# Kernel optimization log

Measured on AMD Instinct MI355X. Metric: run time of the kernel, lower is better.

Reference implementation:

```python
import jax, jax.numpy as jnp
import numpy as np

# BERT-base geometry
B, N, H, DH = 4, 512, 12, 64
HID = H * DH            # 768
E = 65536               # total edges (~avg degree 32)
NREL = 64               # relation vocabulary


def setup_inputs() -> dict:
    key = jax.random.key(0)
    ks = jax.random.split(key, 12)
    node_states = jax.random.normal(ks[0], (B, N, HID), jnp.float32)
    b = jax.random.randint(ks[1], (E,), 0, B)
    hn = jax.random.randint(ks[2], (E,), 0, N)
    tn = jax.random.randint(ks[3], (E,), 0, N)
    r = jax.random.randint(ks[4], (E,), 0, NREL)
    edge_indices = jnp.stack([b, hn, tn, r]).astype(jnp.int32)  # (4, E)
    node_type_ids = jnp.zeros((B, N), jnp.int32)  # unused by this subclass
    sc = 0.02
    Wq = jax.random.normal(ks[5], (HID, HID), jnp.float32) * sc
    bq = jnp.zeros((HID,), jnp.float32)
    Wk = jax.random.normal(ks[6], (HID, HID), jnp.float32) * sc
    bk = jnp.zeros((HID,), jnp.float32)
    Wv = jax.random.normal(ks[7], (HID, HID), jnp.float32) * sc
    bv = jnp.zeros((HID,), jnp.float32)
    # relation matrix embeddings: one (DH, DH) matrix per relation id
    rel_emb = jnp.eye(DH, dtype=jnp.float32)[None] + jax.random.normal(ks[8], (NREL, DH, DH), jnp.float32) * sc
    return {"node_states": node_states, "edge_indices": edge_indices,
            "node_type_ids": node_type_ids, "Wq": Wq, "bq": bq,
            "Wk": Wk, "bk": bk, "Wv": Wv, "bv": bv, "rel_emb": rel_emb}


def reference(node_states, edge_indices, node_type_ids, Wq, bq, Wk, bk, Wv, bv, rel_emb):
    Bq, Nn, hid = node_states.shape
    # dense QKV projections (torch Linear: y = x @ W^T + b)
    Q = node_states @ Wq.T + bq
    K = node_states @ Wk.T + bk
    V = (node_states @ Wv.T + bv).reshape(Bq, Nn, H, DH)  # (B,N,H,D)
    be, he, te, re = edge_indices  # each (E,)
    # per-edge gathers
    Qe = Q[be, he].reshape(-1, H, DH)   # (E,H,D)
    Ke = K[be, te].reshape(-1, H, DH)   # (E,H,D)
    Re = rel_emb[re]                     # (E,D,D) relation matrix per edge
    # Q projected through relation matrix, then inner product with K per head
    Qp = jnp.einsum('ehd,edk->ehk', Qe, Re)
    logits = jnp.einsum('ehd,ehd->eh', Qp, Ke) / jnp.sqrt(jnp.float32(DH))  # (E,H)
    # sparse softmax over tail nodes: segment = (batch, head_node)
    seg = be * Nn + he
    nseg = Bq * Nn
    m = jax.ops.segment_max(logits, seg, num_segments=nseg)      # (BN,H)
    ex = jnp.exp(logits - m[seg])
    denom = jax.ops.segment_sum(ex, seg, num_segments=nseg)      # (BN,H)
    p = ex / denom[seg]                                          # (E,H)
    # dropout prob = 0.0 (deterministic reference)
    # aggregate: out[b,i,h,:] = sum_edges p_e * V[b, tail_e, h, :]
    contrib = p[:, :, None] * V[be, te]                          # (E,H,D)
    out = jax.ops.segment_sum(contrib, seg, num_segments=nseg)   # (BN,H,D)
    return out.reshape(Bq, Nn, H * DH)
```

## Files before the change

### kernel.cpp

```cpp
#include <hip/hip_runtime.h>
#include <hip/hip_bf16.h>

#define NB   4
#define NN   512
#define NH   12
#define DHD  64
#define HID  768
#define NE   65536
#define NSEG 2048
#define NREL 64
#define NSUB 32
#define NRSUB (NREL * NSUB)
#define LGS  16

typedef short bf16x8 __attribute__((ext_vector_type(8)));
typedef float f32x4  __attribute__((ext_vector_type(4)));
typedef unsigned short u16x8 __attribute__((ext_vector_type(8)));

__device__ __forceinline__ unsigned short f2bf(float f) {
    __hip_bfloat16 h = __float2bfloat16(f);
    return *reinterpret_cast<unsigned short*>(&h);
}
__device__ __forceinline__ float bf2f(unsigned short s) {
    return __int_as_float(((int)s) << 16);
}
__device__ __forceinline__ void load_lds16(const void* g, void* l) {
    __builtin_amdgcn_global_load_lds(
        (const __attribute__((address_space(1))) unsigned int*)g,
        (__attribute__((address_space(3))) unsigned int*)l, 16, 0, 0);
}

__global__ __launch_bounds__(256) void zero_kernel(int* __restrict__ counters)
{
    ((int4*)counters)[blockIdx.x * 256 + threadIdx.x] = (int4){0, 0, 0, 0};
}

#define NX4 ((2048 * 768) / 4)
#define NW4 ((768 * 768) / 4)
#define NCAST ((NX4 + 3 * NW4) / 256)
__global__ __launch_bounds__(256) void cast_hist_kernel(
    const float* __restrict__ X, const float* __restrict__ Wq,
    const float* __restrict__ Wk, const float* __restrict__ Wv,
    unsigned short* __restrict__ Xh, unsigned short* __restrict__ Wh,
    const int* __restrict__ ei,
    int* __restrict__ count, int* __restrict__ rcount2)
{
    if (blockIdx.x >= NCAST) {
        const int e = (blockIdx.x - NCAST) * 256 + threadIdx.x;
        const int b  = ei[e];
        const int hn = ei[NE + e];
        const int rr = ei[3 * NE + e];
        const int sub = (e >> 8) & (NSUB - 1);
        atomicAdd(&count[b * NN + hn], 1);
        atomicAdd(&rcount2[rr * NSUB + sub], 1);
        return;
    }
    const int i = blockIdx.x * 256 + threadIdx.x;
    float4 v;
    ushort4* dst;
    if (i < NX4) {
        v = ((const float4*)X)[i];
        dst = &((ushort4*)Xh)[i];
    } else {
        const int j = i - NX4;
        const float* W = (j < NW4) ? Wq : ((j < 2 * NW4) ? Wk : Wv);
        const int jj = (j < NW4) ? j : ((j < 2 * NW4) ? j - NW4 : j - 2 * NW4);
        v = ((const float4*)W)[jj];
        dst = &((ushort4*)Wh)[j];
    }
    ushort4 r;
    r.x = f2bf(v.x); r.y = f2bf(v.y); r.z = f2bf(v.z); r.w = f2bf(v.w);
    *dst = r;
}

__global__ __launch_bounds__(256) void qkv_mfma(
    const unsigned short* __restrict__ Xh, const unsigned short* __restrict__ Wh,
    const float* __restrict__ bq, const float* __restrict__ bk,
    const float* __restrict__ bv,
    unsigned short* __restrict__ Qh, unsigned short* __restrict__ Kh,
    float* __restrict__ Vo)
{
    const int z = blockIdx.z;
    const unsigned short* W = Wh + (size_t)z * (768 * 768);
    const float* bias = (z == 0) ? bq : ((z == 1) ? bk : bv);

    const int n0 = blockIdx.x * 128;
    const int m0 = blockIdx.y * 64;
    const int tid  = threadIdx.x;
    const int lane = tid & 63;
    const int wave = tid >> 6;
    const int wm = wave >> 1, wn = wave & 1;

    __shared__ __align__(16) char smem[64 * 132 * 4];
    unsigned short* As = (unsigned short*)smem;
    unsigned short* Bs = (unsigned short*)(smem + 8192);
    float* Cs = (float*)smem;

    f32x4 acc[2][4];
    #pragma unroll
    for (int a = 0; a < 2; ++a)
        #pragma unroll
        for (int b = 0; b < 4; ++b) acc[a][b] = (f32x4){0.f, 0.f, 0.f, 0.f};

    const int ml = lane & 15;
    const int q4 = lane >> 4;

    for (int k0 = 0; k0 < HID; k0 += 64) {
        __syncthreads();
        #pragma unroll
        for (int i = 0; i < 2; ++i) {
            const int slotb = i * 256 + wave * 64;
            const int idx = slotb + lane;
            const int row = idx >> 3;
            const int kq  = (idx & 7) ^ (row & 7);
            load_lds16(Xh + (size_t)(m0 + row) * HID + k0 + kq * 8,
                       As + slotb * 8);
        }
        #pragma unroll
        for (int i = 0; i < 4; ++i) {
            const int slotb = i * 256 + wave * 64;
            const int idx = slotb + lane;
            const int row = idx >> 3;
            const int kq  = (idx & 7) ^ (row & 7);
            load_lds16(W + (size_t)(n0 + row) * HID + k0 + kq * 8,
                       Bs + slotb * 8);
        }
        __syncthreads();

        #pragma unroll
        for (int ks = 0; ks < 2; ++ks) {
            bf16x8 af[2], bfr[4];
            #pragma unroll
            for (int t = 0; t < 2; ++t) {
                const int ar = wm * 32 + t * 16 + ml;
                const int ac = (ks * 4 + q4) ^ (ar & 7);
                af[t] = *(const bf16x8*)(As + ar * 64 + ac * 8);
            }
            #pragma unroll
            for (int t = 0; t < 4; ++t) {
                const int br = wn * 64 + t * 16 + ml;
                const int bc = (ks * 4 + q4) ^ (br & 7);
                bfr[t] = *(const bf16x8*)(Bs + br * 64 + bc * 8);
            }
            #pragma unroll
            for (int mt = 0; mt < 2; ++mt)
                #pragma unroll
                for (int nt = 0; nt < 4; ++nt)
                    acc[mt][nt] = __builtin_amdgcn_mfma_f32_16x16x32_bf16(
                        af[mt], bfr[nt], acc[mt][nt], 0, 0, 0);
        }
    }

    __syncthreads();
    #pragma unroll
    for (int mt = 0; mt < 2; ++mt)
        #pragma unroll
        for (int nt = 0; nt < 4; ++nt)
            #pragma unroll
            for (int rg = 0; rg < 4; ++rg)
                Cs[(wm * 32 + mt * 16 + q4 * 4 + rg) * 132 +
                   wn * 64 + nt * 16 + ml] = acc[mt][nt][rg];
    __syncthreads();

    #pragma unroll
    for (int it = 0; it < 4; ++it) {
        const int id  = tid + it * 256;
        const int row = id >> 4;
        const int cg  = id & 15;
        const float* cp = Cs + row * 132 + cg * 8;
        const float4 cA = *(const float4*)cp;
        const float4 cB = *(const float4*)(cp + 4);
        const float* bp = bias + n0 + cg * 8;
        const float4 bA = *(const float4*)bp;
        const float4 bB = *(const float4*)(bp + 4);
        const size_t o = (size_t)(m0 + row) * HID + n0 + cg * 8;
        if (z == 2) {
            float4 rA, rB;
            rA.x = cA.x + bA.x; rA.y = cA.y + bA.y;
            rA.z = cA.z + bA.z; rA.w = cA.w + bA.w;
            rB.x = cB.x + bB.x; rB.y = cB.y + bB.y;
            rB.z = cB.z + bB.z; rB.w = cB.w + bB.w;
            *(float4*)&Vo[o]     = rA;
            *(float4*)&Vo[o + 4] = rB;
        } else {
            u16x8 r;
            r[0] = f2bf(cA.x + bA.x); r[1] = f2bf(cA.y + bA.y);
            r[2] = f2bf(cA.z + bA.z); r[3] = f2bf(cA.w + bA.w);
            r[4] = f2bf(cB.x + bB.x); r[5] = f2bf(cB.y + bB.y);
            r[6] = f2bf(cB.z + bB.z); r[7] = f2bf(cB.w + bB.w);
            unsigned short* Y = (z == 0) ? Qh : Kh;
            *(u16x8*)&Y[o] = r;
        }
    }
}

__global__ void scan2_kernel(const int* __restrict__ cntA, int* __restrict__ ofsA,
                             const int* __restrict__ cntB, int* __restrict__ ofsB)
{
    const int* cnt = blockIdx.x ? cntB : cntA;
    int* ofs       = blockIdx.x ? ofsB : ofsA;
    __shared__ int buf[256];
    const int tid = threadIdx.x;
    int local[8];
    int s = 0;
    #pragma unroll
    for (int i = 0; i < 8; ++i) { local[i] = cnt[tid * 8 + i]; s += local[i]; }
    buf[tid] = s;
    __syncthreads();
    for (int off = 1; off < 256; off <<= 1) {
        const int v = (tid >= off) ? buf[tid - off] : 0;
        __syncthreads();
        buf[tid] += v;
        __syncthreads();
    }
    int run = buf[tid] - s;
    #pragma unroll
    for (int i = 0; i < 8; ++i) { ofs[tid * 8 + i] = run; run += local[i]; }
    if (tid == 255) ofs[2048] = run;
}

__global__ void scatter_kernel(const int* __restrict__ ei, const int* __restrict__ offs,
                               int* __restrict__ cursor,
                               const int* __restrict__ rofs2, int* __restrict__ rcursor2,
                               int* __restrict__ s_te, int* __restrict__ s_seg,
                               int* __restrict__ r_pos)
{
    const int e = blockIdx.x * 256 + threadIdx.x;
    const int b  = ei[e];
    const int hn = ei[NE + e];
    const int tn = ei[2 * NE + e];
    const int rr = ei[3 * NE + e];
    const int sub = (e >> 8) & (NSUB - 1);
    const int seg = b * NN + hn;
    const int pos = offs[seg] + atomicAdd(&cursor[seg], 1);
    s_te[pos]  = tn;
    s_seg[pos] = seg;
    const int rb = rr * NSUB + sub;
    const int rj = atomicAdd(&rcursor2[rb], 1);
    r_pos[rofs2[rb] + rj] = pos;
}

#define RLY 32
__global__ __launch_bounds__(256) void rel_logits(
    const unsigned short* __restrict__ Qh, const unsigned short* __restrict__ Kh,
    const float* __restrict__ rel,
    const int* __restrict__ rofs2, const int* __restrict__ r_pos,
    const int* __restrict__ s_te, const int* __restrict__ s_seg,
    float* __restrict__ Lg)
{
    const int r = blockIdx.x;
    const int rstart = rofs2[r * NSUB];
    const int rows = (rofs2[(r + 1) * NSUB] - rstart) * NH;
    if ((int)blockIdx.y * 256 >= rows) return;
    const int tid = threadIdx.x;
    const int lane = tid & 63;
    const int wave = tid >> 6;

    __shared__ int qb[256], kb[256], oi[256];
    __shared__ float QpS[4][16][68];

    bf16x8 bfrag[2][4];
    {
        const float* Rg = rel + (size_t)r * 4096;
        const int q4 = lane >> 4, n = lane & 15;
        #pragma unroll
        for (int ks = 0; ks < 2; ++ks)
            #pragma unroll
            for (int nt = 0; nt < 4; ++nt) {
                bf16x8 f;
                #pragma unroll
                for (int j = 0; j < 8; ++j)
                    f[j] = (short)f2bf(Rg[(ks * 32 + q4 * 8 + j) * 64 + nt * 16 + n]);
                bfrag[ks][nt] = f;
            }
    }

    for (int t0 = blockIdx.y * 256; t0 < rows; t0 += RLY * 256) {
        __syncthreads();
        {
            const int rowid = t0 + tid;
            if (rowid < rows) {
                const int el = rowid / 12;
                const int h  = rowid - el * 12;
                const int pos = r_pos[rstart + el];
                const int seg = s_seg[pos];
                const int te  = s_te[pos];
                const int b   = seg >> 9;
                qb[tid] = seg * HID + h * 64;
                kb[tid] = (b * NN + te) * HID + h * 64;
                oi[tid] = pos * LGS + h;
            } else { qb[tid] = 0; kb[tid] = 0; oi[tid] = -1; }
        }
        __syncthreads();

        for (int g = wave; g < 16; g += 4) {
            const int m = lane & 15, q4 = lane >> 4;
            const int qbase = qb[g * 16 + m];
            f32x4 cfr[4] = {{0,0,0,0},{0,0,0,0},{0,0,0,0},{0,0,0,0}};
            #pragma unroll
            for (int ks = 0; ks < 2; ++ks) {
                const bf16x8 afr = *(const bf16x8*)(Qh + qbase + ks * 32 + q4 * 8);
                #pragma unroll
                for (int nt = 0; nt < 4; ++nt)
                    cfr[nt] = __builtin_amdgcn_mfma_f32_16x16x32_bf16(
                        afr, bfrag[ks][nt], cfr[nt], 0, 0, 0);
            }
            #pragma unroll
            for (int nt = 0; nt < 4; ++nt)
                #pragma unroll
                for (int rg = 0; rg < 4; ++rg)
                    QpS[wave][q4 * 4 + rg][nt * 16 + m] = cfr[nt][rg];

            const int rw = lane >> 2, ch = (lane & 3) * 16;
            const int rowid2 = g * 16 + rw;
            const int kbase = kb[rowid2];
            const bf16x8 k0 = *(const bf16x8*)(Kh + kbase + ch);
            const bf16x8 k1 = *(const bf16x8*)(Kh + kbase + ch + 8);
            float s = 0.f;
            #pragma unroll
            for (int i = 0; i < 8; ++i) {
                s = fmaf(QpS[wave][rw][ch + i],     bf2f((unsigned short)k0[i]), s);
                s = fmaf(QpS[wave][rw][ch + 8 + i], bf2f((unsigned short)k1[i]), s);
            }
            s += __shfl_xor(s, 1, 64);
            s += __shfl_xor(s, 2, 64);
            if ((lane & 3) == 0) {
                const int o = oi[rowid2];
                if (o >= 0) Lg[o] = s * 0.125f;
            }
        }
    }
}

__global__ __launch_bounds__(256) void seg_softmax_agg(
    const float* __restrict__ V, const float* __restrict__ Lg,
    const int* __restrict__ offs, const int* __restrict__ s_te,
    float* __restrict__ out)
{
    const int seg  = blockIdx.x;
    const int tid  = threadIdx.x;
    const int lane = tid & 63;
    const int w    = tid >> 6;
    const int start = offs[seg];
    const int cnt   = offs[seg + 1] - start;
    const int browbase = seg & ~(NN - 1);

    __shared__ int   te_s[64];
    __shared__ float pv[4][3][64];

    float l0 = 0.f, l1 = 0.f, l2 = 0.f;
    float acc0 = 0.f, acc1 = 0.f, acc2 = 0.f;

    for (int c0 = 0; c0 < cnt; c0 += 64) {
        const int cc = min(64, cnt - c0);
        __syncthreads();
        if (tid < cc) te_s[tid] = s_te[start + c0 + tid];
        __syncthreads();

        float p0 = 0.f, p1 = 0.f, p2 = 0.f;
        if (lane < cc) {
            const float* Lp = Lg + (size_t)(start + c0 + lane) * LGS;
            p0 = __expf(Lp[w]); p1 = __expf(Lp[4 + w]); p2 = __expf(Lp[8 + w]);
        }
        float s0 = p0, s1 = p1, s2 = p2;
        #pragma unroll
        for (int o = 1; o < 64; o <<= 1) {
            s0 += __shfl_xor(s0, o, 64);
            s1 += __shfl_xor(s1, o, 64);
            s2 += __shfl_xor(s2, o, 64);
        }
        l0 += s0; l1 += s1; l2 += s2;
        pv[w][0][lane] = p0; pv[w][1][lane] = p1; pv[w][2][lane] = p2;

        for (int j = 0; j < cc; ++j) {
            const float* __restrict__ Vr =
                V + (size_t)(browbase + te_s[j]) * HID + lane;
            acc0 = fmaf(pv[w][0][j], Vr[w * 64],       acc0);
            acc1 = fmaf(pv[w][1][j], Vr[(4 + w) * 64], acc1);
            acc2 = fmaf(pv[w][2][j], Vr[(8 + w) * 64], acc2);
        }
    }

    float* Yo = out + (size_t)seg * HID;
    Yo[tid]       = (l0 > 0.f) ? acc0 / l0 : 0.f;
    Yo[tid + 256] = (l1 > 0.f) ? acc1 / l1 : 0.f;
    Yo[tid + 512] = (l2 > 0.f) ? acc2 / l2 : 0.f;
}

extern "C" void kernel_launch(void* const* d_in, const int* in_sizes, int n_in,
                              void* d_out, int out_size, void* d_ws, size_t ws_size,
                              hipStream_t stream)
{
    const float* X   = (const float*)d_in[0];
    const int*   EI  = (const int*)d_in[1];
    const float* Wq  = (const float*)d_in[3];
    const float* bq  = (const float*)d_in[4];
    const float* Wk  = (const float*)d_in[5];
    const float* bk  = (const float*)d_in[6];
    const float* Wv  = (const float*)d_in[7];
    const float* bv  = (const float*)d_in[8];
    const float* rel = (const float*)d_in[9];
    float* out = (float*)d_out;

    char* p = (char*)d_ws;
    unsigned short* Qh = (unsigned short*)p;  p += (size_t)NSEG * HID * 2;
    unsigned short* Kh = (unsigned short*)p;  p += (size_t)NSEG * HID * 2;
    float* Vb = (float*)p;                    p += (size_t)NSEG * HID * 4;
    unsigned short* Xh = (unsigned short*)p;
    float* Lg = (float*)p;                    p += (size_t)NE * LGS * 4;
    unsigned short* Wh = (unsigned short*)p;  p += (size_t)3 * 768 * 768 * 2;
    int* offs     = (int*)p;                  p += 2052 * 4;
    int* rofs2    = (int*)p;                  p += (NRSUB + 4) * 4;
    int* count    = (int*)p;                  p += NSEG * 4;
    int* cursor   = (int*)p;                  p += NSEG * 4;
    int* rcount2  = (int*)p;                  p += NRSUB * 4;
    int* rcursor2 = (int*)p;                  p += NRSUB * 4;
    int* s_te     = (int*)p;                  p += NE * 4;
    int* s_seg    = (int*)p;                  p += NE * 4;
    int* r_pos    = (int*)p;                  p += NE * 4;

    zero_kernel<<<8, 256, 0, stream>>>(count);
    cast_hist_kernel<<<NCAST + 256, 256, 0, stream>>>(
        X, Wq, Wk, Wv, Xh, Wh, EI, count, rcount2);
    qkv_mfma<<<dim3(HID / 128, (NB * NN) / 64, 3), 256, 0, stream>>>(
        Xh, Wh, bq, bk, bv, Qh, Kh, Vb);

    scan2_kernel<<<2, 256, 0, stream>>>(count, offs, rcount2, rofs2);
    scatter_kernel<<<NE / 256, 256, 0, stream>>>(EI, offs, cursor, rofs2, rcursor2,
                                                 s_te, s_seg, r_pos);

    rel_logits<<<dim3(NREL, RLY), 256, 0, stream>>>(Qh, Kh, rel, rofs2, r_pos,
                                                    s_te, s_seg, Lg);
    seg_softmax_agg<<<NSEG, 256, 0, stream>>>(Vb, Lg, offs, s_te, out);
}
```

Baseline: 176.3 us.

## Fuse prefix scan into scatter, pack seg/tail indices, move exp into logits

Removes the separate two-block scan launch. Every scatter block now recomputes both prefix scans redundantly in shared memory, and block 0 writes the offsets to global memory for later kernels. The per-edge segment and tail indices are packed into one int, so rel_logits does a single gather instead of two. The exp of the logit moves from the softmax kernel into rel_logits. Exponentials are still taken without subtracting the segment max, as before. The cost is 256 blocks each repeating two 2048-entry scans with many barriers, in exchange for one fewer launch and fewer dependent loads.

```diff
diff --git a/kernel.cpp b/kernel.cpp
--- a/kernel.cpp
+++ b/kernel.cpp
@@ -194,50 +194,80 @@
     }
 }
 
-__global__ void scan2_kernel(const int* __restrict__ cntA, int* __restrict__ ofsA,
-                             const int* __restrict__ cntB, int* __restrict__ ofsB)
-{
-    const int* cnt = blockIdx.x ? cntB : cntA;
-    int* ofs       = blockIdx.x ? ofsB : ofsA;
+__global__ __launch_bounds__(256) void scatter_scan_kernel(
+    const int* __restrict__ ei,
+    const int* __restrict__ count, const int* __restrict__ rcount2,
+    int* __restrict__ cursor, int* __restrict__ rcursor2,
+    int* __restrict__ s_te, int* __restrict__ s_pk, int* __restrict__ r_pos,
+    int* __restrict__ offs_g, int* __restrict__ rofs2_g)
+{
+    __shared__ int offs_l[NSEG];
+    __shared__ int rofs_l[NRSUB];
     __shared__ int buf[256];
+    __shared__ int totA;
     const int tid = threadIdx.x;
-    int local[8];
-    int s = 0;
-    #pragma unroll
-    for (int i = 0; i < 8; ++i) { local[i] = cnt[tid * 8 + i]; s += local[i]; }
-    buf[tid] = s;
+
+    {
+        int local[8];
+        int s = 0;
+        #pragma unroll
+        for (int i = 0; i < 8; ++i) { local[i] = count[tid * 8 + i]; s += local[i]; }
+        buf[tid] = s;
+        __syncthreads();
+        for (int off = 1; off < 256; off <<= 1) {
+            const int v = (tid >= off) ? buf[tid - off] : 0;
+            __syncthreads();
+            buf[tid] += v;
+            __syncthreads();
+        }
+        int run = buf[tid] - s;
+        #pragma unroll
+        for (int i = 0; i < 8; ++i) { offs_l[tid * 8 + i] = run; run += local[i]; }
+        if (tid == 255) totA = run;
+        __syncthreads();
+    }
+    {
+        int local[8];
+        int s = 0;
+        #pragma unroll
+        for (int i = 0; i < 8; ++i) { local[i] = rcount2[tid * 8 + i]; s += local[i]; }
+        buf[tid] = s;
+        __syncthreads();
+        for (int off = 1; off < 256; off <<= 1) {
+            const int v = (tid >= off) ? buf[tid - off] : 0;
+            __syncthreads();
+            buf[tid] += v;
+            __syncthreads();
+        }
+        int run = buf[tid] - s;
+        #pragma unroll
+        for (int i = 0; i < 8; ++i) { rofs_l[tid * 8 + i] = run; run += local[i]; }
+        if (blockIdx.x == 0 && tid == 255) rofs2_g[NRSUB] = run;
+    }
     __syncthreads();
-    for (int off = 1; off < 256; off <<= 1) {
-        const int v = (tid >= off) ? buf[tid - off] : 0;
-        __syncthreads();
-        buf[tid] += v;
-        __syncthreads();
-    }
-    int run = buf[tid] - s;
-    #pragma unroll
-    for (int i = 0; i < 8; ++i) { ofs[tid * 8 + i] = run; run += local[i]; }
-    if (tid == 255) ofs[2048] = run;
-}
-
-__global__ void scatter_kernel(const int* __restrict__ ei, const int* __restrict__ offs,
-                               int* __restrict__ cursor,
-                               const int* __restrict__ rofs2, int* __restrict__ rcursor2,
-                               int* __restrict__ s_te, int* __restrict__ s_seg,
-                               int* __restrict__ r_pos)
-{
-    const int e = blockIdx.x * 256 + threadIdx.x;
+
+    if (blockIdx.x == 0) {
+        #pragma unroll
+        for (int i = 0; i < 8; ++i) {
+            offs_g[tid * 8 + i]  = offs_l[tid * 8 + i];
+            rofs2_g[tid * 8 + i] = rofs_l[tid * 8 + i];
+        }
+        if (tid == 255) offs_g[NSEG] = totA;
+    }
+
+    const int e = blockIdx.x * 256 + tid;
     const int b  = ei[e];
     const int hn = ei[NE + e];
     const int tn = ei[2 * NE + e];
     const int rr = ei[3 * NE + e];
     const int sub = (e >> 8) & (NSUB - 1);
     const int seg = b * NN + hn;
-    const int pos = offs[seg] + atomicAdd(&cursor[seg], 1);
-    s_te[pos]  = tn;
-    s_seg[pos] = seg;
+    const int pos = offs_l[seg] + atomicAdd(&cursor[seg], 1);
+    s_te[pos] = tn;
+    s_pk[pos] = (seg << 9) | tn;
     const int rb = rr * NSUB + sub;
     const int rj = atomicAdd(&rcursor2[rb], 1);
-    r_pos[rofs2[rb] + rj] = pos;
+    r_pos[rofs_l[rb] + rj] = pos;
 }
 
 #define RLY 32
@@ -245,7 +275,7 @@
     const unsigned short* __restrict__ Qh, const unsigned short* __restrict__ Kh,
     const float* __restrict__ rel,
     const int* __restrict__ rofs2, const int* __restrict__ r_pos,
-    const int* __restrict__ s_te, const int* __restrict__ s_seg,
+    const int* __restrict__ s_pk,
     float* __restrict__ Lg)
 {
     const int r = blockIdx.x;
@@ -283,11 +313,11 @@
                 const int el = rowid / 12;
                 const int h  = rowid - el * 12;
                 const int pos = r_pos[rstart + el];
-                const int seg = s_seg[pos];
-                const int te  = s_te[pos];
-                const int b   = seg >> 9;
+                const int pk  = s_pk[pos];
+                const int seg = pk >> 9;
+                const int te  = pk & (NN - 1);
                 qb[tid] = seg * HID + h * 64;
-                kb[tid] = (b * NN + te) * HID + h * 64;
+                kb[tid] = ((seg & ~(NN - 1)) + te) * HID + h * 64;
                 oi[tid] = pos * LGS + h;
             } else { qb[tid] = 0; kb[tid] = 0; oi[tid] = -1; }
         }
@@ -326,7 +356,7 @@
             s += __shfl_xor(s, 2, 64);
             if ((lane & 3) == 0) {
                 const int o = oi[rowid2];
-                if (o >= 0) Lg[o] = s * 0.125f;
+                if (o >= 0) Lg[o] = __expf(s * 0.125f);
             }
         }
     }
@@ -360,7 +390,7 @@
         float p0 = 0.f, p1 = 0.f, p2 = 0.f;
         if (lane < cc) {
             const float* Lp = Lg + (size_t)(start + c0 + lane) * LGS;
-            p0 = __expf(Lp[w]); p1 = __expf(Lp[4 + w]); p2 = __expf(Lp[8 + w]);
+            p0 = Lp[w]; p1 = Lp[4 + w]; p2 = Lp[8 + w];
         }
         float s0 = p0, s1 = p1, s2 = p2;
         #pragma unroll
@@ -416,7 +446,7 @@
     int* rcount2  = (int*)p;                  p += NRSUB * 4;
     int* rcursor2 = (int*)p;                  p += NRSUB * 4;
     int* s_te     = (int*)p;                  p += NE * 4;
-    int* s_seg    = (int*)p;                  p += NE * 4;
+    int* s_pk     = (int*)p;                  p += NE * 4;
     int* r_pos    = (int*)p;                  p += NE * 4;
 
     zero_kernel<<<8, 256, 0, stream>>>(count);
@@ -425,11 +455,10 @@
     qkv_mfma<<<dim3(HID / 128, (NB * NN) / 64, 3), 256, 0, stream>>>(
         Xh, Wh, bq, bk, bv, Qh, Kh, Vb);
 
-    scan2_kernel<<<2, 256, 0, stream>>>(count, offs, rcount2, rofs2);
-    scatter_kernel<<<NE / 256, 256, 0, stream>>>(EI, offs, cursor, rofs2, rcursor2,
-                                                 s_te, s_seg, r_pos);
+    scatter_scan_kernel<<<NE / 256, 256, 0, stream>>>(
+        EI, count, rcount2, cursor, rcursor2, s_te, s_pk, r_pos, offs, rofs2);
 
     rel_logits<<<dim3(NREL, RLY), 256, 0, stream>>>(Qh, Kh, rel, rofs2, r_pos,
-                                                    s_te, s_seg, Lg);
+                                                    s_pk, Lg);
     seg_softmax_agg<<<NSEG, 256, 0, stream>>>(Vb, Lg, offs, s_te, out);
 }
```

New measurement: 173.6 us. Within noise of the previous version (-1.5%).
